# Kernel tuning notes

Hardware: AMD Instinct MI355X
Metric: run time of the kernel (lower is better)

## Reference

```python
import jax, jax.numpy as jnp
import numpy as np

RADIUS = 0.2
OC = 128   # output_channel
EC = 64    # extra_input_channel


def _select(radius, xyz):
    # xyz: [BT, N, 3] -> idx [BT, N, 8] (nearest point in each octant within radius, else self)
    BT, N, _ = xyz.shape
    jd = radius * radius
    diff = xyz[:, None, :, :] - xyz[:, :, None, :]          # diff[b, n, j] = xyz[b, j] - xyz[b, n]
    dist = jnp.sum(diff * diff, -1)                          # [BT, N, N]
    # torch .int() truncates toward zero; jnp float->int32 cast does the same
    octant = jnp.sum((diff + 1.0).astype(jnp.int32) *
                     jnp.array([4, 2, 1], jnp.int32), -1)    # [BT, N, N]
    eye = jnp.arange(N)
    # self entry gets judge_dist (fallback winner), everything else 1e10
    base = jnp.where(eye[:, None] == eye[None, :],
                     jnp.float32(jd), jnp.float32(1e10))[None]  # [1, N, N]
    valid = (dist > 1e-10) & (dist < jd)
    idx8 = [jnp.argmin(jnp.where((octant == i) & valid, dist, base), -1)
            for i in range(8)]
    return jnp.stack(idx8, -1)                               # [BT, N, 8]


def _gather(p, idx):
    # p: [BT, N, C], idx: [BT, N, 8] -> [BT, N, 8, C]
    return jax.vmap(lambda a, i: a[i])(p, idx)


def _conv12(x, w, b):
    # Conv2d kernel [1,2] stride [1,2]: x [B, C, N, W] -> [B, O, N, W//2]
    B_, C, N, Wd = x.shape
    xp = x.reshape(B_, C, N, Wd // 2, 2)
    return jnp.einsum('bcnpk,ock->bonp', xp, w) + b[None, :, None, None]


def _forward(xyz4, points4, w1a, b1a, w1b, b1b, w1c, b1c, w2a, b2a, w2b, b2b, w2c, b2c):
    B, T, N, _ = xyz4.shape
    xyz = xyz4.reshape(B * T, N, 3)
    pts = points4.reshape(B * T, N, -1)
    idx = _select(RADIUS, xyz)
    g_xyz = _gather(xyz, idx) - xyz[:, :, None, :]           # [BT, N, 8, 3]
    g_pts = jnp.concatenate([g_xyz, _gather(pts, idx)], -1)  # [BT, N, 8, 3+EC]
    x = g_pts.transpose(0, 3, 1, 2)                          # [BT, C, N, 8]
    x = _conv12(x, w1a, b1a)
    x = _conv12(x, w1b, b1b)
    x = _conv12(x, w1c, b1c)                                 # [BT, OC, N, 1]
    new = x[..., 0].transpose(0, 2, 1)                       # [BT, N, OC]
    g_pts2 = jnp.concatenate([g_xyz, _gather(new, idx)], -1) # [BT, N, 8, 3+OC]
    x = g_pts2.transpose(0, 3, 1, 2)
    x = _conv12(x, w2a, b2a)
    x = _conv12(x, w2b, b2b)
    x = _conv12(x, w2c, b2c)                                 # [BT, OC, N, 1]
    new = x[..., 0]                                          # [BT, OC, N]
    out = jnp.concatenate([new, pts.transpose(0, 2, 1)], 1)  # merge='concat'
    out = jax.nn.relu(out).transpose(0, 2, 1).reshape(B, T, N, -1)
    return xyz4, out


def setup_inputs() -> dict:
    key = jax.random.key(0)
    ks = jax.random.split(key, 16)
    B, T, N = 4, 4, 1024
    xyz = jax.random.uniform(ks[0], (B, T, N, 3), jnp.float32)
    points = jax.random.normal(ks[1], (B, T, N, EC), jnp.float32)
    w = lambda k, o, c: jax.random.normal(k, (o, c, 2), jnp.float32) * 0.05
    b = lambda k, o: jax.random.normal(k, (o,), jnp.float32) * 0.05
    return {
        'xyz': xyz, 'points': points,
        'w1a': w(ks[2], OC, 3 + EC), 'b1a': b(ks[3], OC),
        'w1b': w(ks[4], OC, OC),     'b1b': b(ks[5], OC),
        'w1c': w(ks[6], OC, OC),     'b1c': b(ks[7], OC),
        'w2a': w(ks[8], OC, 3 + OC), 'b2a': b(ks[9], OC),
        'w2b': w(ks[10], OC, OC),    'b2b': b(ks[11], OC),
        'w2c': w(ks[12], OC, OC),    'b2c': b(ks[13], OC),
    }


def reference(xyz, points, w1a, b1a, w1b, b1b, w1c, b1c, w2a, b2a, w2b, b2b, w2c, b2c):
    return _forward(xyz, points, w1a, b1a, w1b, b1b, w1c, b1c,
                    w2a, b2a, w2b, b2b, w2c, b2c)
```

## Files before the change

### kernel.cpp

```cpp
#include <hip/hip_runtime.h>
#include <stdint.h>

typedef unsigned int u32;
typedef unsigned long long u64;
typedef unsigned short us;
using short8 = __attribute__((ext_vector_type(8))) short;
using us8    = __attribute__((ext_vector_type(8))) us;
using f32x4  = __attribute__((ext_vector_type(4))) float;

#define BT 16
#define NPT 1024

__device__ __forceinline__ us f2bf(float f) {
    u32 u = __float_as_uint(f);
    u += 0x7fffu + ((u >> 16) & 1u);
    return (us)(u >> 16);
}
__device__ __forceinline__ float bf2f(us v) { return __uint_as_float(((u32)v) << 16); }
__device__ __forceinline__ u32 packbf(float lo, float hi) {
    return (u32)f2bf(lo) | ((u32)f2bf(hi) << 16);
}

__device__ void wprep_a(int tid, const float* __restrict__ w, us* __restrict__ dst,
                        int Cfeat, int Creal, int NOCT) {
    int lane = tid & 63, ct = (tid >> 6) & 7, kt = tid >> 9;
    int o = ct * 16 + (lane & 15);
    int h = lane >> 4;
    int ci = kt * 4 + h;
    int p = (ci >= NOCT) ? 1 : 0;
    int q = ci - p * NOCT;
    us8 v;
#pragma unroll
    for (int j = 0; j < 8; ++j) {
        int c = q * 8 + j;
        int ref = (c < Cfeat) ? c + 3 : ((c < Cfeat + 3) ? c - Cfeat : -1);
        v[j] = (ref >= 0) ? f2bf(w[((size_t)o * Creal + ref) * 2 + p]) : (us)0;
    }
    *(us8*)(dst + (size_t)tid * 8) = v;
}

__device__ void wprep_b(int tid, const float* __restrict__ w, us* __restrict__ dst) {
    int lane = tid & 63, ct = (tid >> 6) & 7, kt = tid >> 9;
    int o = ct * 16 + (lane & 15);
    int k0 = kt * 32 + ((lane >> 4) << 3);
    us8 v;
#pragma unroll
    for (int j = 0; j < 8; ++j) v[j] = f2bf(w[(size_t)o * 256 + k0 + j]);
    *(us8*)(dst + (size_t)tid * 8) = v;
}

__global__ __launch_bounds__(256) void k_prep(
    const float* __restrict__ xyz, const float* __restrict__ pts,
    const float* __restrict__ w1a, us* __restrict__ f1a,
    const float* __restrict__ w1b, us* __restrict__ f1b,
    const float* __restrict__ w1c, us* __restrict__ f1c,
    const float* __restrict__ w2a, us* __restrict__ f2a,
    const float* __restrict__ w2b, us* __restrict__ f2b,
    const float* __restrict__ w2c, us* __restrict__ f2c,
    us* __restrict__ ptsbf, us* __restrict__ newbf, float* __restrict__ outp) {
    const int u2 = blockIdx.x, t = threadIdx.x;
    if (u2 < 92) {
        if (u2 < 10)      wprep_a(u2 * 256 + t, w1a, f1a, 64, 67, 10);
        else if (u2 < 26) wprep_b((u2 - 10) * 256 + t, w1b, f1b);
        else if (u2 < 42) wprep_b((u2 - 26) * 256 + t, w1c, f1c);
        else if (u2 < 60) wprep_a((u2 - 42) * 256 + t, w2a, f2a, 128, 131, 18);
        else if (u2 < 76) wprep_b((u2 - 60) * 256 + t, w2b, f2b);
        else              wprep_b((u2 - 76) * 256 + t, w2c, f2c);
    } else if (u2 < 140) {
        int id = (u2 - 92) * 256 + t;
        ((float4*)outp)[id] = ((const float4*)xyz)[id];
    } else if (u2 < 204) {
        int r = (u2 - 140) * 256 + t;
        const float4* pr = (const float4*)(pts + ((size_t)r << 6));
        u32* dst = (u32*)(ptsbf + (size_t)r * 80);
#pragma unroll
        for (int i = 0; i < 16; ++i) {
            float4 f = pr[i];
            dst[2 * i]     = packbf(f.x, f.y);
            dst[2 * i + 1] = packbf(f.z, f.w);
        }
        const float* xr = xyz + (size_t)r * 3;
        dst[32] = packbf(xr[0], xr[1]);
        dst[33] = packbf(xr[2], 0.f);
#pragma unroll
        for (int i = 34; i < 40; ++i) dst[i] = 0u;
    } else {
        int r = (u2 - 204) * 256 + t;
        u32* dst = (u32*)(newbf + (size_t)r * 144);
        const float* xr = xyz + (size_t)r * 3;
        dst[64] = packbf(xr[0], xr[1]);
        dst[65] = packbf(xr[2], 0.f);
#pragma unroll
        for (int i = 66; i < 72; ++i) dst[i] = 0u;
    }
}

__global__ __launch_bounds__(256) void k_s1(
    const float* __restrict__ xyz, const us* __restrict__ ptsbf,
    u64* __restrict__ keys,
    const us* __restrict__ wfa, const float* __restrict__ ba,
    const us* __restrict__ wfb, const float* __restrict__ bb,
    const us* __restrict__ wfc, const float* __restrict__ bc,
    us* __restrict__ newbf_out) {
    constexpr int KTA = 5, NOCT = 10, RSTR = 80, FIXC = 64, FIXQ = 8;
    __shared__ __align__(16) char smem[24576];
    __shared__ u64 kfin[16][8];
    __shared__ float snn[48];
    us* abuf = (us*)smem;
    us* cbuf = (us*)(smem + 16384);

    const int u = (int)(((blockIdx.x & 7u) << 7) | (blockIdx.x >> 3));
    const int t = threadIdx.x, wid = t >> 6, lane = t & 63;
    const int li = lane & 15, h = lane >> 4;
    const int g0 = u * 16;
    const int b = u >> 6;
    const int nb0 = g0 & (NPT - 1);
    const float* xg = xyz + (size_t)b * 3072;
    const us* fb = ptsbf + (size_t)b * NPT * RSTR;

    const int j0 = (wid << 8) + (lane << 2);
    float4 c0 = *(const float4*)(xg + (size_t)j0 * 3);
    float4 c1 = *(const float4*)(xg + (size_t)j0 * 3 + 4);
    float4 c2 = *(const float4*)(xg + (size_t)j0 * 3 + 8);
    const float jxc[4] = {c0.x, c0.w, c1.z, c2.y};
    const float jyc[4] = {c0.y, c1.x, c1.w, c2.z};
    const float jzc[4] = {c0.z, c1.y, c2.x, c2.w};

    if (t < 48) snn[t] = xg[(size_t)nb0 * 3 + t];
    if (t < 128)
        kfin[t >> 3][t & 7] = ((u64)__float_as_uint(0.04f) << 32) | (u32)(nb0 + (t >> 3));
    __syncthreads();

    for (int i = 0; i < 16; ++i) {
        const float xn = snn[i * 3], yn = snn[i * 3 + 1], zn = snn[i * 3 + 2];
#pragma unroll
        for (int jj = 0; jj < 4; ++jj) {
            float dx = __fadd_rn(jxc[jj], -xn);
            float dy = __fadd_rn(jyc[jj], -yn);
            float dz = __fadd_rn(jzc[jj], -zn);
            float d = __fadd_rn(__fadd_rn(__fmul_rn(dx, dx), __fmul_rn(dy, dy)),
                                __fmul_rn(dz, dz));
            if (d > 1e-10f && d < 0.04f) {
                int oct = ((int)__fadd_rn(dx, 1.0f)) * 4 + ((int)__fadd_rn(dy, 1.0f)) * 2 +
                          ((int)__fadd_rn(dz, 1.0f));
                u64 key = ((u64)__float_as_uint(d) << 32) | (u32)(j0 + jj);
                atomicMin(&kfin[i][oct], key);
            }
        }
    }
    __syncthreads();

    if (t < 128)
        keys[(((size_t)g0 + (t >> 3)) << 3) + (t & 7)] = kfin[t >> 3][t & 7];
    const int n_loc_c = wid * 4 + (li >> 2), pos = li & 3;
    const int J0 = (int)(u32)kfin[n_loc_c][2 * pos];
    const int J1 = (int)(u32)kfin[n_loc_c][2 * pos + 1];
    const int N = nb0 + n_loc_c;
    __syncthreads();

    const us* row0 = fb + (size_t)J0 * RSTR;
    const us* row1 = fb + (size_t)J1 * RSTR;
    us8 xn8 = *(const us8*)(fb + (size_t)N * RSTR + FIXC);
    const float xn0 = bf2f(xn8[0]), xn1 = bf2f(xn8[1]), xn2 = bf2f(xn8[2]);

    f32x4 acc[8];
#pragma unroll
    for (int ct = 0; ct < 8; ++ct) {
        float bv = ba[ct * 16 + li];
        acc[ct] = f32x4{bv, bv, bv, bv};
    }
    for (int kt = 0; kt < KTA; ++kt) {
        int ci = kt * 4 + h;
        int q = (ci >= NOCT) ? ci - NOCT : ci;
        const us* rp = (ci >= NOCT) ? row1 : row0;
        us8 v = *(const us8*)(rp + q * 8);
        if (q == FIXQ) {
            v[0] = f2bf(__fadd_rn(bf2f(v[0]), -xn0));
            v[1] = f2bf(__fadd_rn(bf2f(v[1]), -xn1));
            v[2] = f2bf(__fadd_rn(bf2f(v[2]), -xn2));
        }
        short8 a = __builtin_bit_cast(short8, v);
        const us* wk = wfa + (size_t)kt * 4096;
#pragma unroll
        for (int ct = 0; ct < 8; ++ct) {
            short8 w = *(const short8*)(wk + ((size_t)ct * 64 + lane) * 8);
            acc[ct] = __builtin_amdgcn_mfma_f32_16x16x32_bf16(a, w, acc[ct], 0, 0, 0);
        }
    }
    {
        u32* dst = (u32*)abuf;
        int mbase = wid * 16 + (h << 2);
        int mr0 = mbase >> 1, mr1 = mr0 + 1;
#pragma unroll
        for (int ct = 0; ct < 8; ++ct) {
            f32x4 av = acc[ct];
            u32 p0 = packbf(av[0], av[1]);
            u32 p1 = packbf(av[2], av[3]);
            dst[((mr0 >> 4) * 8 + ct) * 256 + ((mr0 & 15) + ((li >> 2) << 4)) * 4 + (li & 3)] = p0;
            dst[((mr1 >> 4) * 8 + ct) * 256 + ((mr1 & 15) + ((li >> 2) << 4)) * 4 + (li & 3)] = p1;
        }
    }
    __syncthreads();

    const int mtB = wid >> 1, ctbB = (wid & 1) * 4;
    f32x4 accB[4];
#pragma unroll
    for (int cc = 0; cc < 4; ++cc) {
        float bv = bb[(ctbB + cc) * 16 + li];
        accB[cc] = f32x4{bv, bv, bv, bv};
    }
    for (int kt = 0; kt < 8; ++kt) {
        short8 a = *(const short8*)(abuf + (((size_t)mtB * 8 + kt) * 64 + lane) * 8);
        const us* wk = wfb + ((size_t)kt * 8 + ctbB) * 512;
#pragma unroll
        for (int cc = 0; cc < 4; ++cc) {
            short8 w = *(const short8*)(wk + ((size_t)cc * 64 + lane) * 8);
            accB[cc] = __builtin_amdgcn_mfma_f32_16x16x32_bf16(a, w, accB[cc], 0, 0, 0);
        }
    }
    {
        u32* dst = (u32*)cbuf;
        int mbase = mtB * 16 + (h << 2);
        int mr0 = mbase >> 1, mr1 = mr0 + 1;
#pragma unroll
        for (int cc = 0; cc < 4; ++cc) {
            int ct = ctbB + cc;
            f32x4 av = accB[cc];
            u32 p0 = packbf(av[0], av[1]);
            u32 p1 = packbf(av[2], av[3]);
            dst[ct * 256 + (mr0 + ((li >> 2) << 4)) * 4 + (li & 3)] = p0;
            dst[ct * 256 + (mr1 + ((li >> 2) << 4)) * 4 + (li & 3)] = p1;
        }
    }
    __syncthreads();

    f32x4 accC[2];
#pragma unroll
    for (int cc = 0; cc < 2; ++cc) {
        float bv = bc[(wid * 2 + cc) * 16 + li];
        accC[cc] = f32x4{bv, bv, bv, bv};
    }
    for (int kt = 0; kt < 8; ++kt) {
        short8 a = *(const short8*)(cbuf + ((size_t)kt * 64 + lane) * 8);
        const us* wk = wfc + ((size_t)kt * 8 + wid * 2) * 512;
#pragma unroll
        for (int cc = 0; cc < 2; ++cc) {
            short8 w = *(const short8*)(wk + ((size_t)cc * 64 + lane) * 8);
            accC[cc] = __builtin_amdgcn_mfma_f32_16x16x32_bf16(a, w, accC[cc], 0, 0, 0);
        }
    }
#pragma unroll
    for (int cc = 0; cc < 2; ++cc) {
        int o = (wid * 2 + cc) * 16 + li;
#pragma unroll
        for (int r = 0; r < 4; ++r) {
            int gg = g0 + h * 4 + r;
            newbf_out[(size_t)gg * 144 + o] = f2bf(accC[cc][r]);
        }
    }
}

__global__ __launch_bounds__(256) void k_s2(
    const float* __restrict__ pts, const us* __restrict__ feat,
    const u32* __restrict__ keys32,
    const us* __restrict__ wfa, const float* __restrict__ ba,
    const us* __restrict__ wfb, const float* __restrict__ bb,
    const us* __restrict__ wfc, const float* __restrict__ bc,
    float* __restrict__ outp) {
    constexpr int KTA = 9, NOCT = 18, RSTR = 144, FIXC = 128, FIXQ = 16;
    __shared__ us abuf[2 * 8 * 512];
    __shared__ us cbuf[1 * 8 * 512];

    const int u = (int)(((blockIdx.x & 7u) << 7) | (blockIdx.x >> 3));
    const int t = threadIdx.x, wid = t >> 6, lane = t & 63;
    const int li = lane & 15, h = lane >> 4;
    const int m0 = u * 64;
    const int g0 = u * 16;
    const int b = u >> 6;
    const us* fb = feat + (size_t)b * NPT * RSTR;

    const int m = m0 + wid * 16 + li;
    const int g = m >> 2, pos = m & 3;
    const int J0 = (int)keys32[((size_t)g * 8 + 2 * pos) * 2];
    const int J1 = (int)keys32[((size_t)g * 8 + 2 * pos + 1) * 2];
    const int N = g & (NPT - 1);

    const us* row0 = fb + (size_t)J0 * RSTR;
    const us* row1 = fb + (size_t)J1 * RSTR;
    us8 xn8 = *(const us8*)(fb + (size_t)N * RSTR + FIXC);
    const float xn0 = bf2f(xn8[0]), xn1 = bf2f(xn8[1]), xn2 = bf2f(xn8[2]);

    f32x4 acc[8];
#pragma unroll
    for (int ct = 0; ct < 8; ++ct) {
        float bv = ba[ct * 16 + li];
        acc[ct] = f32x4{bv, bv, bv, bv};
    }
    for (int kt = 0; kt < KTA; ++kt) {
        int ci = kt * 4 + h;
        int q = (ci >= NOCT) ? ci - NOCT : ci;
        const us* rp = (ci >= NOCT) ? row1 : row0;
        us8 v = *(const us8*)(rp + q * 8);
        if (q == FIXQ) {
            v[0] = f2bf(__fadd_rn(bf2f(v[0]), -xn0));
            v[1] = f2bf(__fadd_rn(bf2f(v[1]), -xn1));
            v[2] = f2bf(__fadd_rn(bf2f(v[2]), -xn2));
        }
        short8 a = __builtin_bit_cast(short8, v);
        const us* wk = wfa + (size_t)kt * 4096;
#pragma unroll
        for (int ct = 0; ct < 8; ++ct) {
            short8 w = *(const short8*)(wk + ((size_t)ct * 64 + lane) * 8);
            acc[ct] = __builtin_amdgcn_mfma_f32_16x16x32_bf16(a, w, acc[ct], 0, 0, 0);
        }
    }
    {
        u32* dst = (u32*)abuf;
        int mbase = wid * 16 + (h << 2);
        int mr0 = mbase >> 1, mr1 = mr0 + 1;
#pragma unroll
        for (int ct = 0; ct < 8; ++ct) {
            f32x4 av = acc[ct];
            u32 p0 = packbf(av[0], av[1]);
            u32 p1 = packbf(av[2], av[3]);
            dst[((mr0 >> 4) * 8 + ct) * 256 + ((mr0 & 15) + ((li >> 2) << 4)) * 4 + (li & 3)] = p0;
            dst[((mr1 >> 4) * 8 + ct) * 256 + ((mr1 & 15) + ((li >> 2) << 4)) * 4 + (li & 3)] = p1;
        }
    }
    __syncthreads();

    const int mtB = wid >> 1, ctbB = (wid & 1) * 4;
    f32x4 accB[4];
#pragma unroll
    for (int cc = 0; cc < 4; ++cc) {
        float bv = bb[(ctbB + cc) * 16 + li];
        accB[cc] = f32x4{bv, bv, bv, bv};
    }
    for (int kt = 0; kt < 8; ++kt) {
        short8 a = *(const short8*)(abuf + (((size_t)mtB * 8 + kt) * 64 + lane) * 8);
        const us* wk = wfb + ((size_t)kt * 8 + ctbB) * 512;
#pragma unroll
        for (int cc = 0; cc < 4; ++cc) {
            short8 w = *(const short8*)(wk + ((size_t)cc * 64 + lane) * 8);
            accB[cc] = __builtin_amdgcn_mfma_f32_16x16x32_bf16(a, w, accB[cc], 0, 0, 0);
        }
    }
    {
        u32* dst = (u32*)cbuf;
        int mbase = mtB * 16 + (h << 2);
        int mr0 = mbase >> 1, mr1 = mr0 + 1;
#pragma unroll
        for (int cc = 0; cc < 4; ++cc) {
            int ct = ctbB + cc;
            f32x4 av = accB[cc];
            u32 p0 = packbf(av[0], av[1]);
            u32 p1 = packbf(av[2], av[3]);
            dst[ct * 256 + (mr0 + ((li >> 2) << 4)) * 4 + (li & 3)] = p0;
            dst[ct * 256 + (mr1 + ((li >> 2) << 4)) * 4 + (li & 3)] = p1;
        }
    }
    __syncthreads();

    f32x4 accC[2];
#pragma unroll
    for (int cc = 0; cc < 2; ++cc) {
        float bv = bc[(wid * 2 + cc) * 16 + li];
        accC[cc] = f32x4{bv, bv, bv, bv};
    }
    for (int kt = 0; kt < 8; ++kt) {
        short8 a = *(const short8*)(cbuf + ((size_t)kt * 64 + lane) * 8);
        const us* wk = wfc + ((size_t)kt * 8 + wid * 2) * 512;
#pragma unroll
        for (int cc = 0; cc < 2; ++cc) {
            short8 w = *(const short8*)(wk + ((size_t)cc * 64 + lane) * 8);
            accC[cc] = __builtin_amdgcn_mfma_f32_16x16x32_bf16(a, w, accC[cc], 0, 0, 0);
        }
    }
#pragma unroll
    for (int cc = 0; cc < 2; ++cc) {
        int o = (wid * 2 + cc) * 16 + li;
#pragma unroll
        for (int r = 0; r < 4; ++r) {
            int gg = g0 + h * 4 + r;
            outp[(size_t)49152 + (size_t)gg * 192 + o] = fmaxf(accC[cc][r], 0.f);
        }
    }

    {
        int r = t >> 4, q = t & 15;
        float4 v = ((const float4*)(pts + ((size_t)(g0 + r) << 6)))[q];
        v.x = fmaxf(v.x, 0.0f);
        v.y = fmaxf(v.y, 0.0f);
        v.z = fmaxf(v.z, 0.0f);
        v.w = fmaxf(v.w, 0.0f);
        *(float4*)(outp + 49152 + (size_t)(g0 + r) * 192 + 128 + q * 4) = v;
    }
}

extern "C" void kernel_launch(void* const* d_in, const int* in_sizes, int n_in,
                              void* d_out, int out_size, void* d_ws, size_t ws_size,
                              hipStream_t stream) {
    const float* xyz = (const float*)d_in[0];
    const float* pts = (const float*)d_in[1];
    const float* w1a = (const float*)d_in[2];
    const float* b1a = (const float*)d_in[3];
    const float* w1b = (const float*)d_in[4];
    const float* b1b = (const float*)d_in[5];
    const float* w1c = (const float*)d_in[6];
    const float* b1c = (const float*)d_in[7];
    const float* w2a = (const float*)d_in[8];
    const float* b2a = (const float*)d_in[9];
    const float* w2b = (const float*)d_in[10];
    const float* b2b = (const float*)d_in[11];
    const float* w2c = (const float*)d_in[12];
    const float* b2c = (const float*)d_in[13];
    float* outp = (float*)d_out;

    char* ws = (char*)d_ws;
    u64* keys = (u64*)ws;
    const u32* keys32 = (const u32*)ws;
    us* wf1a = (us*)(ws + 1048576);
    us* wf1b = (us*)(ws + 1089536);
    us* wf1c = (us*)(ws + 1155072);
    us* wf2a = (us*)(ws + 1220608);
    us* wf2b = (us*)(ws + 1294336);
    us* wf2c = (us*)(ws + 1359872);
    us* ptsbf = (us*)(ws + 2097152);
    us* newbf = (us*)(ws + 5242880);

    k_prep<<<268, 256, 0, stream>>>(xyz, pts, w1a, wf1a, w1b, wf1b, w1c, wf1c,
                                    w2a, wf2a, w2b, wf2b, w2c, wf2c,
                                    ptsbf, newbf, outp);
    k_s1<<<1024, 256, 0, stream>>>(xyz, ptsbf, keys,
                                   wf1a, b1a, wf1b, b1b, wf1c, b1c, newbf);
    k_s2<<<1024, 256, 0, stream>>>(pts, newbf, keys32,
                                   wf2a, b2a, wf2b, b2b, wf2c, b2c, outp);
}
```

Before: 53.11 us.

## Fuse three kernels into one cooperative persistent kernel with grid syncs

Merges the prep, stage-1 and stage-2 kernels into a single cooperative launch that loops over work units and uses grid-wide barriers between phases. The launch is sized from the occupancy query (capped at 1024 blocks), and the old three-launch path is kept as a fallback if the cooperative launch fails. The aim is to remove per-launch overhead and the gaps between kernels. In exchange it adds grid.sync costs, per-call occupancy queries on the host, and possibly lower occupancy from the shared-memory union, since k_s2 no longer gets its own smaller footprint.

Measured after the change: 55.49 us. 1.04x slower.

```diff
diff --git a/kernel.cpp b/kernel.cpp
--- a/kernel.cpp
+++ b/kernel.cpp
@@ -1,5 +1,8 @@
 #include <hip/hip_runtime.h>
+#include <hip/hip_cooperative_groups.h>
 #include <stdint.h>
+
+namespace cg = cooperative_groups;
 
 typedef unsigned int u32;
 typedef unsigned long long u64;
@@ -10,6 +13,15 @@
 
 #define BT 16
 #define NPT 1024
+
+struct Params {
+    const float *xyz, *pts;
+    const float *w1a, *b1a, *w1b, *b1b, *w1c, *b1c;
+    const float *w2a, *b2a, *w2b, *b2b, *w2c, *b2c;
+    u64* keys;
+    us *wf1a, *wf1b, *wf1c, *wf2a, *wf2b, *wf2c, *ptsbf, *newbf;
+    float* outp;
+};
 
 __device__ __forceinline__ us f2bf(float f) {
     u32 u = __float_as_uint(f);
@@ -49,45 +61,37 @@
     *(us8*)(dst + (size_t)tid * 8) = v;
 }
 
-__global__ __launch_bounds__(256) void k_prep(
-    const float* __restrict__ xyz, const float* __restrict__ pts,
-    const float* __restrict__ w1a, us* __restrict__ f1a,
-    const float* __restrict__ w1b, us* __restrict__ f1b,
-    const float* __restrict__ w1c, us* __restrict__ f1c,
-    const float* __restrict__ w2a, us* __restrict__ f2a,
-    const float* __restrict__ w2b, us* __restrict__ f2b,
-    const float* __restrict__ w2c, us* __restrict__ f2c,
-    us* __restrict__ ptsbf, us* __restrict__ newbf, float* __restrict__ outp) {
-    const int u2 = blockIdx.x, t = threadIdx.x;
+__device__ void prep_unit(int u2, const Params& p) {
+    const int t = threadIdx.x;
     if (u2 < 92) {
-        if (u2 < 10)      wprep_a(u2 * 256 + t, w1a, f1a, 64, 67, 10);
-        else if (u2 < 26) wprep_b((u2 - 10) * 256 + t, w1b, f1b);
-        else if (u2 < 42) wprep_b((u2 - 26) * 256 + t, w1c, f1c);
-        else if (u2 < 60) wprep_a((u2 - 42) * 256 + t, w2a, f2a, 128, 131, 18);
-        else if (u2 < 76) wprep_b((u2 - 60) * 256 + t, w2b, f2b);
-        else              wprep_b((u2 - 76) * 256 + t, w2c, f2c);
+        if (u2 < 10)      wprep_a(u2 * 256 + t, p.w1a, p.wf1a, 64, 67, 10);
+        else if (u2 < 26) wprep_b((u2 - 10) * 256 + t, p.w1b, p.wf1b);
+        else if (u2 < 42) wprep_b((u2 - 26) * 256 + t, p.w1c, p.wf1c);
+        else if (u2 < 60) wprep_a((u2 - 42) * 256 + t, p.w2a, p.wf2a, 128, 131, 18);
+        else if (u2 < 76) wprep_b((u2 - 60) * 256 + t, p.w2b, p.wf2b);
+        else              wprep_b((u2 - 76) * 256 + t, p.w2c, p.wf2c);
     } else if (u2 < 140) {
         int id = (u2 - 92) * 256 + t;
-        ((float4*)outp)[id] = ((const float4*)xyz)[id];
+        ((float4*)p.outp)[id] = ((const float4*)p.xyz)[id];
     } else if (u2 < 204) {
         int r = (u2 - 140) * 256 + t;
-        const float4* pr = (const float4*)(pts + ((size_t)r << 6));
-        u32* dst = (u32*)(ptsbf + (size_t)r * 80);
+        const float4* pr = (const float4*)(p.pts + ((size_t)r << 6));
+        u32* dst = (u32*)(p.ptsbf + (size_t)r * 80);
 #pragma unroll
         for (int i = 0; i < 16; ++i) {
             float4 f = pr[i];
             dst[2 * i]     = packbf(f.x, f.y);
             dst[2 * i + 1] = packbf(f.z, f.w);
         }
-        const float* xr = xyz + (size_t)r * 3;
+        const float* xr = p.xyz + (size_t)r * 3;
         dst[32] = packbf(xr[0], xr[1]);
         dst[33] = packbf(xr[2], 0.f);
 #pragma unroll
         for (int i = 34; i < 40; ++i) dst[i] = 0u;
     } else {
         int r = (u2 - 204) * 256 + t;
-        u32* dst = (u32*)(newbf + (size_t)r * 144);
-        const float* xr = xyz + (size_t)r * 3;
+        u32* dst = (u32*)(p.newbf + (size_t)r * 144);
+        const float* xr = p.xyz + (size_t)r * 3;
         dst[64] = packbf(xr[0], xr[1]);
         dst[65] = packbf(xr[2], 0.f);
 #pragma unroll
@@ -95,28 +99,20 @@
     }
 }
 
-__global__ __launch_bounds__(256) void k_s1(
-    const float* __restrict__ xyz, const us* __restrict__ ptsbf,
-    u64* __restrict__ keys,
-    const us* __restrict__ wfa, const float* __restrict__ ba,
-    const us* __restrict__ wfb, const float* __restrict__ bb,
-    const us* __restrict__ wfc, const float* __restrict__ bc,
-    us* __restrict__ newbf_out) {
+__device__ void s1_unit(int uraw, const Params& p, char* smem, u64 (*kfin)[8],
+                        float* snn) {
     constexpr int KTA = 5, NOCT = 10, RSTR = 80, FIXC = 64, FIXQ = 8;
-    __shared__ __align__(16) char smem[24576];
-    __shared__ u64 kfin[16][8];
-    __shared__ float snn[48];
     us* abuf = (us*)smem;
     us* cbuf = (us*)(smem + 16384);
 
-    const int u = (int)(((blockIdx.x & 7u) << 7) | (blockIdx.x >> 3));
+    const int u = (int)((((u32)uraw & 7u) << 7) | ((u32)uraw >> 3));
     const int t = threadIdx.x, wid = t >> 6, lane = t & 63;
     const int li = lane & 15, h = lane >> 4;
     const int g0 = u * 16;
     const int b = u >> 6;
     const int nb0 = g0 & (NPT - 1);
-    const float* xg = xyz + (size_t)b * 3072;
-    const us* fb = ptsbf + (size_t)b * NPT * RSTR;
+    const float* xg = p.xyz + (size_t)b * 3072;
+    const us* fb = p.ptsbf + (size_t)b * NPT * RSTR;
 
     const int j0 = (wid << 8) + (lane << 2);
     float4 c0 = *(const float4*)(xg + (size_t)j0 * 3);
@@ -126,6 +122,7 @@
     const float jyc[4] = {c0.y, c1.x, c1.w, c2.z};
     const float jzc[4] = {c0.z, c1.y, c2.x, c2.w};
 
+    __syncthreads();
     if (t < 48) snn[t] = xg[(size_t)nb0 * 3 + t];
     if (t < 128)
         kfin[t >> 3][t & 7] = ((u64)__float_as_uint(0.04f) << 32) | (u32)(nb0 + (t >> 3));
@@ -151,7 +148,7 @@
     __syncthreads();
 
     if (t < 128)
-        keys[(((size_t)g0 + (t >> 3)) << 3) + (t & 7)] = kfin[t >> 3][t & 7];
+        p.keys[(((size_t)g0 + (t >> 3)) << 3) + (t & 7)] = kfin[t >> 3][t & 7];
     const int n_loc_c = wid * 4 + (li >> 2), pos = li & 3;
     const int J0 = (int)(u32)kfin[n_loc_c][2 * pos];
     const int J1 = (int)(u32)kfin[n_loc_c][2 * pos + 1];
@@ -166,7 +163,7 @@
     f32x4 acc[8];
 #pragma unroll
     for (int ct = 0; ct < 8; ++ct) {
-        float bv = ba[ct * 16 + li];
+        float bv = p.b1a[ct * 16 + li];
         acc[ct] = f32x4{bv, bv, bv, bv};
     }
     for (int kt = 0; kt < KTA; ++kt) {
@@ -180,7 +177,7 @@
             v[2] = f2bf(__fadd_rn(bf2f(v[2]), -xn2));
         }
         short8 a = __builtin_bit_cast(short8, v);
-        const us* wk = wfa + (size_t)kt * 4096;
+        const us* wk = p.wf1a + (size_t)kt * 4096;
 #pragma unroll
         for (int ct = 0; ct < 8; ++ct) {
             short8 w = *(const short8*)(wk + ((size_t)ct * 64 + lane) * 8);
@@ -206,12 +203,12 @@
     f32x4 accB[4];
 #pragma unroll
     for (int cc = 0; cc < 4; ++cc) {
-        float bv = bb[(ctbB + cc) * 16 + li];
+        float bv = p.b1b[(ctbB + cc) * 16 + li];
         accB[cc] = f32x4{bv, bv, bv, bv};
     }
     for (int kt = 0; kt < 8; ++kt) {
         short8 a = *(const short8*)(abuf + (((size_t)mtB * 8 + kt) * 64 + lane) * 8);
-        const us* wk = wfb + ((size_t)kt * 8 + ctbB) * 512;
+        const us* wk = p.wf1b + ((size_t)kt * 8 + ctbB) * 512;
 #pragma unroll
         for (int cc = 0; cc < 4; ++cc) {
             short8 w = *(const short8*)(wk + ((size_t)cc * 64 + lane) * 8);
@@ -237,12 +234,12 @@
     f32x4 accC[2];
 #pragma unroll
     for (int cc = 0; cc < 2; ++cc) {
-        float bv = bc[(wid * 2 + cc) * 16 + li];
+        float bv = p.b1c[(wid * 2 + cc) * 16 + li];
         accC[cc] = f32x4{bv, bv, bv, bv};
     }
     for (int kt = 0; kt < 8; ++kt) {
         short8 a = *(const short8*)(cbuf + ((size_t)kt * 64 + lane) * 8);
-        const us* wk = wfc + ((size_t)kt * 8 + wid * 2) * 512;
+        const us* wk = p.wf1c + ((size_t)kt * 8 + wid * 2) * 512;
 #pragma unroll
         for (int cc = 0; cc < 2; ++cc) {
             short8 w = *(const short8*)(wk + ((size_t)cc * 64 + lane) * 8);
@@ -255,29 +252,24 @@
 #pragma unroll
         for (int r = 0; r < 4; ++r) {
             int gg = g0 + h * 4 + r;
-            newbf_out[(size_t)gg * 144 + o] = f2bf(accC[cc][r]);
-        }
-    }
-}
-
-__global__ __launch_bounds__(256) void k_s2(
-    const float* __restrict__ pts, const us* __restrict__ feat,
-    const u32* __restrict__ keys32,
-    const us* __restrict__ wfa, const float* __restrict__ ba,
-    const us* __restrict__ wfb, const float* __restrict__ bb,
-    const us* __restrict__ wfc, const float* __restrict__ bc,
-    float* __restrict__ outp) {
+            p.newbf[(size_t)gg * 144 + o] = f2bf(accC[cc][r]);
+        }
+    }
+}
+
+__device__ void s2_unit(int uraw, const Params& p, char* smem) {
     constexpr int KTA = 9, NOCT = 18, RSTR = 144, FIXC = 128, FIXQ = 16;
-    __shared__ us abuf[2 * 8 * 512];
-    __shared__ us cbuf[1 * 8 * 512];
-
-    const int u = (int)(((blockIdx.x & 7u) << 7) | (blockIdx.x >> 3));
+    us* abuf = (us*)smem;
+    us* cbuf = (us*)(smem + 16384);
+    const u32* keys32 = (const u32*)p.keys;
+
+    const int u = (int)((((u32)uraw & 7u) << 7) | ((u32)uraw >> 3));
     const int t = threadIdx.x, wid = t >> 6, lane = t & 63;
     const int li = lane & 15, h = lane >> 4;
     const int m0 = u * 64;
     const int g0 = u * 16;
     const int b = u >> 6;
-    const us* fb = feat + (size_t)b * NPT * RSTR;
+    const us* fb = p.newbf + (size_t)b * NPT * RSTR;
 
     const int m = m0 + wid * 16 + li;
     const int g = m >> 2, pos = m & 3;
@@ -290,10 +282,12 @@
     us8 xn8 = *(const us8*)(fb + (size_t)N * RSTR + FIXC);
     const float xn0 = bf2f(xn8[0]), xn1 = bf2f(xn8[1]), xn2 = bf2f(xn8[2]);
 
+    __syncthreads();
+
     f32x4 acc[8];
 #pragma unroll
     for (int ct = 0; ct < 8; ++ct) {
-        float bv = ba[ct * 16 + li];
+        float bv = p.b2a[ct * 16 + li];
         acc[ct] = f32x4{bv, bv, bv, bv};
     }
     for (int kt = 0; kt < KTA; ++kt) {
@@ -307,7 +301,7 @@
             v[2] = f2bf(__fadd_rn(bf2f(v[2]), -xn2));
         }
         short8 a = __builtin_bit_cast(short8, v);
-        const us* wk = wfa + (size_t)kt * 4096;
+        const us* wk = p.wf2a + (size_t)kt * 4096;
 #pragma unroll
         for (int ct = 0; ct < 8; ++ct) {
             short8 w = *(const short8*)(wk + ((size_t)ct * 64 + lane) * 8);
@@ -333,12 +327,12 @@
     f32x4 accB[4];
 #pragma unroll
     for (int cc = 0; cc < 4; ++cc) {
-        float bv = bb[(ctbB + cc) * 16 + li];
+        float bv = p.b2b[(ctbB + cc) * 16 + li];
         accB[cc] = f32x4{bv, bv, bv, bv};
     }
     for (int kt = 0; kt < 8; ++kt) {
         short8 a = *(const short8*)(abuf + (((size_t)mtB * 8 + kt) * 64 + lane) * 8);
-        const us* wk = wfb + ((size_t)kt * 8 + ctbB) * 512;
+        const us* wk = p.wf2b + ((size_t)kt * 8 + ctbB) * 512;
 #pragma unroll
         for (int cc = 0; cc < 4; ++cc) {
             short8 w = *(const short8*)(wk + ((size_t)cc * 64 + lane) * 8);
@@ -364,12 +358,12 @@
     f32x4 accC[2];
 #pragma unroll
     for (int cc = 0; cc < 2; ++cc) {
-        float bv = bc[(wid * 2 + cc) * 16 + li];
+        float bv = p.b2c[(wid * 2 + cc) * 16 + li];
         accC[cc] = f32x4{bv, bv, bv, bv};
     }
     for (int kt = 0; kt < 8; ++kt) {
         short8 a = *(const short8*)(cbuf + ((size_t)kt * 64 + lane) * 8);
-        const us* wk = wfc + ((size_t)kt * 8 + wid * 2) * 512;
+        const us* wk = p.wf2c + ((size_t)kt * 8 + wid * 2) * 512;
 #pragma unroll
         for (int cc = 0; cc < 2; ++cc) {
             short8 w = *(const short8*)(wk + ((size_t)cc * 64 + lane) * 8);
@@ -382,57 +376,92 @@
 #pragma unroll
         for (int r = 0; r < 4; ++r) {
             int gg = g0 + h * 4 + r;
-            outp[(size_t)49152 + (size_t)gg * 192 + o] = fmaxf(accC[cc][r], 0.f);
+            p.outp[(size_t)49152 + (size_t)gg * 192 + o] = fmaxf(accC[cc][r], 0.f);
         }
     }
 
     {
         int r = t >> 4, q = t & 15;
-        float4 v = ((const float4*)(pts + ((size_t)(g0 + r) << 6)))[q];
+        float4 v = ((const float4*)(p.pts + ((size_t)(g0 + r) << 6)))[q];
         v.x = fmaxf(v.x, 0.0f);
         v.y = fmaxf(v.y, 0.0f);
         v.z = fmaxf(v.z, 0.0f);
         v.w = fmaxf(v.w, 0.0f);
-        *(float4*)(outp + 49152 + (size_t)(g0 + r) * 192 + 128 + q * 4) = v;
-    }
+        *(float4*)(p.outp + 49152 + (size_t)(g0 + r) * 192 + 128 + q * 4) = v;
+    }
+}
+
+__global__ __launch_bounds__(256) void k_prep(Params p) {
+    prep_unit(blockIdx.x, p);
+}
+__global__ __launch_bounds__(256) void k_s1(Params p) {
+    __shared__ __align__(16) char smem[24576];
+    __shared__ u64 kfin[16][8];
+    __shared__ float snn[48];
+    s1_unit(blockIdx.x, p, smem, kfin, snn);
+}
+__global__ __launch_bounds__(256) void k_s2(Params p) {
+    __shared__ __align__(16) char smem[24576];
+    s2_unit(blockIdx.x, p, smem);
+}
+
+__global__ __launch_bounds__(256) void k_all(Params p) {
+    __shared__ __align__(16) char smem[24576];
+    __shared__ u64 kfin[16][8];
+    __shared__ float snn[48];
+    cg::grid_group grid = cg::this_grid();
+    const int gsz = (int)gridDim.x;
+
+    for (int u = blockIdx.x; u < 268; u += gsz) prep_unit(u, p);
+    grid.sync();
+    for (int u = blockIdx.x; u < 1024; u += gsz) s1_unit(u, p, smem, kfin, snn);
+    grid.sync();
+    for (int u = blockIdx.x; u < 1024; u += gsz) s2_unit(u, p, smem);
 }
 
 extern "C" void kernel_launch(void* const* d_in, const int* in_sizes, int n_in,
                               void* d_out, int out_size, void* d_ws, size_t ws_size,
                               hipStream_t stream) {
-    const float* xyz = (const float*)d_in[0];
-    const float* pts = (const float*)d_in[1];
-    const float* w1a = (const float*)d_in[2];
-    const float* b1a = (const float*)d_in[3];
-    const float* w1b = (const float*)d_in[4];
-    const float* b1b = (const float*)d_in[5];
-    const float* w1c = (const float*)d_in[6];
-    const float* b1c = (const float*)d_in[7];
-    const float* w2a = (const float*)d_in[8];
-    const float* b2a = (const float*)d_in[9];
-    const float* w2b = (const float*)d_in[10];
-    const float* b2b = (const float*)d_in[11];
-    const float* w2c = (const float*)d_in[12];
-    const float* b2c = (const float*)d_in[13];
-    float* outp = (float*)d_out;
-
     char* ws = (char*)d_ws;
-    u64* keys = (u64*)ws;
-    const u32* keys32 = (const u32*)ws;
-    us* wf1a = (us*)(ws + 1048576);
-    us* wf1b = (us*)(ws + 1089536);
-    us* wf1c = (us*)(ws + 1155072);
-    us* wf2a = (us*)(ws + 1220608);
-    us* wf2b = (us*)(ws + 1294336);
-    us* wf2c = (us*)(ws + 1359872);
-    us* ptsbf = (us*)(ws + 2097152);
-    us* newbf = (us*)(ws + 5242880);
-
-    k_prep<<<268, 256, 0, stream>>>(xyz, pts, w1a, wf1a, w1b, wf1b, w1c, wf1c,
-                                    w2a, wf2a, w2b, wf2b, w2c, wf2c,
-                                    ptsbf, newbf, outp);
-    k_s1<<<1024, 256, 0, stream>>>(xyz, ptsbf, keys,
-                                   wf1a, b1a, wf1b, b1b, wf1c, b1c, newbf);
-    k_s2<<<1024, 256, 0, stream>>>(pts, newbf, keys32,
-                                   wf2a, b2a, wf2b, b2b, wf2c, b2c, outp);
-}
+    Params prm;
+    prm.xyz = (const float*)d_in[0];
+    prm.pts = (const float*)d_in[1];
+    prm.w1a = (const float*)d_in[2];  prm.b1a = (const float*)d_in[3];
+    prm.w1b = (const float*)d_in[4];  prm.b1b = (const float*)d_in[5];
+    prm.w1c = (const float*)d_in[6];  prm.b1c = (const float*)d_in[7];
+    prm.w2a = (const float*)d_in[8];  prm.b2a = (const float*)d_in[9];
+    prm.w2b = (const float*)d_in[10]; prm.b2b = (const float*)d_in[11];
+    prm.w2c = (const float*)d_in[12]; prm.b2c = (const float*)d_in[13];
+    prm.keys  = (u64*)ws;
+    prm.wf1a  = (us*)(ws + 1048576);
+    prm.wf1b  = (us*)(ws + 1089536);
+    prm.wf1c  = (us*)(ws + 1155072);
+    prm.wf2a  = (us*)(ws + 1220608);
+    prm.wf2b  = (us*)(ws + 1294336);
+    prm.wf2c  = (us*)(ws + 1359872);
+    prm.ptsbf = (us*)(ws + 2097152);
+    prm.newbf = (us*)(ws + 5242880);
+    prm.outp  = (float*)d_out;
+
+    bool coop_ok = false;
+    int nb = 0;
+    hipError_t qerr = hipOccupancyMaxActiveBlocksPerMultiprocessor(
+        &nb, (const void*)k_all, 256, 0);
+    if (qerr == hipSuccess && nb >= 1) {
+        unsigned grid = (unsigned)nb * 256u;
+        if (grid > 1024u) grid = 1024u;
+        void* args[] = { (void*)&prm };
+        hipError_t lerr = hipLaunchCooperativeKernel((const void*)k_all, dim3(grid),
+                                                     dim3(256), args, 0, stream);
+        if (lerr == hipSuccess) coop_ok = true;
+        else (void)hipGetLastError();
+    } else {
+        (void)hipGetLastError();
+    }
+
+    if (!coop_ok) {
+        k_prep<<<268, 256, 0, stream>>>(prm);
+        k_s1<<<1024, 256, 0, stream>>>(prm);
+        k_s2<<<1024, 256, 0, stream>>>(prm);
+    }
+}
```
